# Performance work log

Measured on AMD Instinct MI355X. Metric: run time of the kernel, lower is better.

## Reference

```python
import jax, jax.numpy as jnp
import numpy as np

B = 262144
STATE_DIM = 12
ACTION_DIM = 1
MSG_DIM = 32
MAX_CHILDREN = 2
EPS = 1e-12  # F.normalize default eps


def _l2norm(x):
    n = jnp.sqrt(jnp.sum(x * x, axis=-1, keepdims=True))
    return x / jnp.maximum(n, EPS)


def setup_inputs() -> dict:
    key = jax.random.key(0)
    ks = jax.random.split(key, 16)

    def lin(kw, kb, out_d, in_d):
        lim = 1.0 / np.sqrt(in_d)
        w = jax.random.uniform(kw, (out_d, in_d), jnp.float32, -lim, lim)
        b = jax.random.uniform(kb, (out_d,), jnp.float32, -lim, lim)
        return w, b

    state = jax.random.normal(ks[0], (B, STATE_DIM), jnp.float32)
    action = jax.random.normal(ks[1], (B, ACTION_DIM), jnp.float32)

    # ModelUp (sNet): fc1, fc2, fc3
    up_w1, up_b1 = lin(ks[2], ks[3], 64, STATE_DIM + ACTION_DIM)
    up_w2, up_b2 = lin(ks[4], ks[5], 64, 64 + MSG_DIM * MAX_CHILDREN)
    up_w3, up_b3 = lin(ks[6], ks[7], MSG_DIM, 64)

    # ModelDownAction.model = MLPBase(msg_dim + action_dim + msg_dim, msg_dim)
    dyn_w1, dyn_b1 = lin(ks[8], ks[9], 400, MSG_DIM + ACTION_DIM + MSG_DIM)
    dyn_w2, dyn_b2 = lin(ks[10], ks[11], 300, 400)
    dyn_w3, dyn_b3 = lin(ks[12], ks[13], MSG_DIM, 300)

    return dict(state=state, action=action,
                up_w1=up_w1, up_b1=up_b1, up_w2=up_w2, up_b2=up_b2,
                up_w3=up_w3, up_b3=up_b3,
                dyn_w1=dyn_w1, dyn_b1=dyn_b1, dyn_w2=dyn_w2, dyn_b2=dyn_b2,
                dyn_w3=dyn_w3, dyn_b3=dyn_b3)


def reference(state, action,
              up_w1, up_b1, up_w2, up_b2, up_w3, up_b3,
              dyn_w1, dyn_b1, dyn_w2, dyn_b2, dyn_w3, dyn_b3):
    # num_limbs == 1, parents = [-1], td = bu = True, disable_fold = True
    x = state                              # (B, state_dim)
    u = action                             # (B, 1)

    # ---- bottom_up_transmission(0): ModelUp with all-zero child messages ----
    m_children = jnp.zeros((B, MSG_DIM * MAX_CHILDREN), x.dtype)
    xu = jnp.concatenate([x, u], axis=-1)
    xu = _l2norm(xu @ up_w1.T + up_b1)                       # (B, 64)
    xum = jnp.tanh(jnp.concatenate([xu, m_children], axis=-1))
    xum = jnp.tanh(xum @ up_w2.T + up_b2)                    # (B, 64)
    msg_up = _l2norm(xum @ up_w3.T + up_b3)                  # (B, msg_dim)

    # ---- top_down_transmission(0): ModelDownAction, state := msg_up ----
    # parent_msg = zeros, self_children_idx = 0 -> msg_in = zeros slice
    msg_in = jnp.zeros((B, MSG_DIM), x.dtype)
    xum2 = jnp.concatenate([msg_up, u, msg_in], axis=-1)     # (B, 2*msg_dim+1)
    h = jax.nn.relu(xum2 @ dyn_w1.T + dyn_b1)                # (B, 400)
    h = jax.nn.relu(h @ dyn_w2.T + dyn_b2)                   # (B, 300)
    delta = h @ dyn_w3.T + dyn_b3                            # (B, msg_dim)

    # stack over num_limbs=1 then squeeze -> (B, msg_dim)
    return delta
```

## Files before the change

kernel.cpp:

```cpp
#include <hip/hip_runtime.h>
#include <stdint.h>

typedef short s16x8 __attribute__((ext_vector_type(8)));
typedef float f32x16 __attribute__((ext_vector_type(16)));
typedef unsigned int u32;
typedef unsigned int u32x2 __attribute__((ext_vector_type(2)));

#define NFRAG 336
#define WS_USHORTS (NFRAG*512)
#define PANEL_FRAGS 14
#define PANEL_BYTES (PANEL_FRAGS*1024)
#define LDS_BYTES (3*PANEL_BYTES)

#define MFMA(a,b,c) __builtin_amdgcn_mfma_f32_32x32x16_bf16((a),(b),(c),0,0,0)

__device__ __forceinline__ unsigned short f2bf(float f){
  u32 x = __builtin_bit_cast(u32, f);
  x += 0x7fffu + ((x >> 16) & 1u);
  return (unsigned short)(x >> 16);
}

__device__ __forceinline__ float bfhi(float b){
  return __builtin_bit_cast(float, (u32)f2bf(b) << 16);
}

__device__ __forceinline__ u32 pkbf(float a, float b){
  u32 r;
  asm("v_cvt_pk_bf16_f32 %0, %1, %2" : "=v"(r) : "v"(a), "v"(b));
  return r;
}

__device__ __forceinline__ float fast_tanh(float x){
  float ax = fabsf(x);
  float e = __expf(-2.0f * ax);
  float r = (1.0f - e) * __builtin_amdgcn_rcpf(1.0f + e);
  return x < 0.0f ? -r : r;
}

__device__ __forceinline__ float halfsum(float s){
  return s + __shfl_xor(s, 32);
}

__device__ __forceinline__ void tile2frags(const f32x16 v, s16x8& f0, s16x8& f1){
  u32 w00 = pkbf(v[0],  v[1]),  w01 = pkbf(v[2],  v[3]);
  u32 w10 = pkbf(v[4],  v[5]),  w11 = pkbf(v[6],  v[7]);
  u32 w20 = pkbf(v[8],  v[9]),  w21 = pkbf(v[10], v[11]);
  u32 w30 = pkbf(v[12], v[13]), w31 = pkbf(v[14], v[15]);
  u32x2 p0 = __builtin_amdgcn_permlane32_swap(w00, w10, false, false);
  u32x2 p1 = __builtin_amdgcn_permlane32_swap(w01, w11, false, false);
  u32x2 p2 = __builtin_amdgcn_permlane32_swap(w20, w30, false, false);
  u32x2 p3 = __builtin_amdgcn_permlane32_swap(w21, w31, false, false);
  int4 r0, r1;
  r0.x = (int)p0[0]; r0.y = (int)p1[0]; r0.z = (int)p0[1]; r0.w = (int)p1[1];
  r1.x = (int)p2[0]; r1.y = (int)p3[0]; r1.z = (int)p2[1]; r1.w = (int)p3[1];
  f0 = __builtin_bit_cast(s16x8, r0);
  f1 = __builtin_bit_cast(s16x8, r1);
}

__global__ void wconv_kernel(const float* __restrict__ uw1, const float* __restrict__ ub1,
                             const float* __restrict__ uw2, const float* __restrict__ ub2,
                             const float* __restrict__ uw3, const float* __restrict__ ub3,
                             const float* __restrict__ dw1, const float* __restrict__ db1,
                             const float* __restrict__ dw2, const float* __restrict__ db2,
                             const float* __restrict__ dw3, const float* __restrict__ db3,
                             unsigned short* __restrict__ wp)
{
  int i = blockIdx.x*256 + threadIdx.x;
  if (i >= WS_USHORTS) return;
  int f    = i >> 9;
  int lane = (i >> 3) & 63;
  int j    = i & 7;
  int row  = lane & 31;
  int k8   = (lane >> 5)*8 + j;
  float v = 0.0f;
  if (f < 2){
    int feat = f*32 + row; int k = k8;
    if (k < 13) v = uw1[feat*13 + k];
    else if (k == 13) v = ub1[feat];
    else if (k == 14) v = ub1[feat] - bfhi(ub1[feat]);
  } else if (f < 12){
    int t = f - 2; int kt = t >> 1, nt = t & 1;
    int feat = nt*32 + row; int k = kt*16 + k8;
    if (k < 64) v = uw2[feat*128 + k];
    else if (k == 64) v = ub2[feat];
    else if (k == 65) v = ub2[feat] - bfhi(ub2[feat]);
  } else if (f < 17){
    int kt = f - 12; int feat = row; int k = kt*16 + k8;
    if (k < 64) v = uw3[feat*64 + k];
    else if (k == 64) v = ub3[feat];
    else if (k == 65) v = ub3[feat] - bfhi(ub3[feat]);
  } else if (f < 56){
    int t = f - 17; int nt = t/3, kt = t%3;
    int feat = nt*32 + row; int k = kt*16 + k8;
    if (feat < 400){
      if (k < 33) v = dw1[feat*65 + k];
      else if (k == 33) v = db1[feat];
      else if (k == 34) v = db1[feat] - bfhi(db1[feat]);
    } else if ((feat == 400 || feat == 401) && k == 33) v = 1.0f;
  } else {
    int t = f - 56; int n = t/56; int r = t%56;
    if (r < 52){
      int kf = r >> 1, nt = r & 1;
      int feat = n*64 + nt*32 + row; int k = kf*16 + k8;
      if (feat < 300){
        if (k < 400) v = dw2[feat*400 + k];
        else if (k == 400) v = db2[feat];
        else if (k == 401) v = db2[feat] - bfhi(db2[feat]);
      } else if ((feat == 300 || feat == 301) && k == 400) v = 1.0f;
    } else {
      int kt = n*4 + (r - 52); int feat = row; int k = kt*16 + k8;
      if (k < 300) v = dw3[feat*300 + k];
      else if (k == 300) v = db3[feat];
      else if (k == 301) v = db3[feat] - bfhi(db3[feat]);
    }
  }
  wp[i] = f2bf(v);
}

__device__ __forceinline__ s16x8 fragF(const char* sm, int f, int ln){
  return *(const s16x8*)(sm + ((f/PANEL_FRAGS) % 3)*PANEL_BYTES
                            + (f % PANEL_FRAGS)*1024 + ln*16);
}

__device__ __forceinline__ void stage14(const unsigned short* wp, char* sm, int panel, int tid){
  char* dst = sm + (panel % 3)*PANEL_BYTES;
  const char* src = (const char*)wp + (size_t)panel*PANEL_BYTES;
  #pragma unroll
  for (int j = 0; j < 3; ++j){
    int off = j*4096 + tid*16;
    __builtin_amdgcn_global_load_lds(
      (const __attribute__((address_space(1))) unsigned int*)(src + off),
      (__attribute__((address_space(3))) unsigned int*)(dst + off), 16, 0, 0);
  }
  int off3 = 12288 + (tid & 127)*16;
  __builtin_amdgcn_global_load_lds(
    (const __attribute__((address_space(1))) unsigned int*)(src + off3),
    (__attribute__((address_space(3))) unsigned int*)(dst + off3), 16, 0, 0);
}

#define BND(P) { \
  if ((P) >= 23) { asm volatile("s_waitcnt vmcnt(0) lgkmcnt(0)" ::: "memory"); } \
  else           { asm volatile("s_waitcnt vmcnt(4) lgkmcnt(0)" ::: "memory"); } \
  __builtin_amdgcn_s_barrier(); \
  __builtin_amdgcn_sched_barrier(0); \
  if ((P)+2 <= 23) stage14(wp, sm, (P)+2, tid); \
}

#define D1TRIPLE(f0_, oA, oB) { \
  f32x16 a = {}; \
  __builtin_amdgcn_s_setprio(1); \
  a = MFMA(fragF(sm, (f0_)+0, ln), mf0, a); \
  a = MFMA(fragF(sm, (f0_)+1, ln), mf1, a); \
  a = MFMA(fragF(sm, (f0_)+2, ln), mf2, a); \
  __builtin_amdgcn_s_setprio(0); \
  _Pragma("unroll") \
  for (int r = 0; r < 16; ++r) a[r] = fmaxf(a[r], 0.f); \
  tile2frags(a, oA, oB); }

#define D2RUN(fb, r0, r1) { \
  __builtin_amdgcn_s_setprio(1); \
  _Pragma("unroll") \
  for (int r = (r0); r < (r1); ++r){ \
    s16x8 hb = h1f[r>>1]; \
    if (r & 1) d2a1 = MFMA(fragF(sm, (fb)+r, ln), hb, d2a1); \
    else       d2a0 = MFMA(fragF(sm, (fb)+r, ln), hb, d2a0); \
  } \
  __builtin_amdgcn_s_setprio(0); }

#define D2TAIL(fb) { \
  _Pragma("unroll") \
  for (int r = 0; r < 16; ++r){ \
    d2a0[r] = fmaxf(d2a0[r], 0.f); \
    d2a1[r] = fmaxf(d2a1[r], 0.f); \
  } \
  s16x8 c0, c1, c2, c3; \
  tile2frags(d2a0, c0, c1); \
  tile2frags(d2a1, c2, c3); \
  __builtin_amdgcn_s_setprio(1); \
  acc3 = MFMA(fragF(sm, (fb)+52, ln), c0, acc3); \
  acc3 = MFMA(fragF(sm, (fb)+53, ln), c1, acc3); \
  acc3 = MFMA(fragF(sm, (fb)+54, ln), c2, acc3); \
  acc3 = MFMA(fragF(sm, (fb)+55, ln), c3, acc3); \
  __builtin_amdgcn_s_setprio(0); }

#define CHUNK(fb, P0) { \
  f32x16 d2a0 = {}, d2a1 = {}; \
  BND(P0) \
  D2RUN(fb, 0, 14) \
  BND((P0)+1) \
  D2RUN(fb, 14, 28) \
  BND((P0)+2) \
  D2RUN(fb, 28, 42) \
  BND((P0)+3) \
  D2RUN(fb, 42, 52) \
  D2TAIL(fb) \
}

__global__ __launch_bounds__(256, 2) void fused_kernel(
    const float* __restrict__ state, const float* __restrict__ action,
    const unsigned short* __restrict__ wp, float* __restrict__ out)
{
  __shared__ __align__(1024) char sm[LDS_BYTES];

  const int tid = threadIdx.x;
  const int ln  = tid & 63;
  const int wid = tid >> 6;
  const int c   = ln & 31;
  const int h   = ln >> 5;
  const int rowb = blockIdx.x*128 + wid*32;

  const float* xr = state + (size_t)(rowb + c)*12;
  float u = action[rowb + c];
  float4 xa, xbr;
  if (h == 0){
    xa  = *(const float4*)xr;
    xbr = *(const float4*)(xr + 4);
  } else {
    xa  = *(const float4*)(xr + 8);
  }

  stage14(wp, sm, 0, tid);
  stage14(wp, sm, 1, tid);
  BND(0)

  float4 xb = (h == 0) ? xbr : float4{u, 1.0f, 1.0f, 0.0f};
  int4 xw;
  xw.x = pkbf(xa.x, xa.y); xw.y = pkbf(xa.z, xa.w);
  xw.z = pkbf(xb.x, xb.y); xw.w = pkbf(xb.z, xb.w);
  s16x8 xfrag = __builtin_bit_cast(s16x8, xw);
  int4 ow = {0,0,0,0}; if (h == 0) ow.x = 0x3F803F80;
  s16x8 onef = __builtin_bit_cast(s16x8, ow);
  int4 mw = {0,0,0,0};
  if (h == 0){ mw.x = pkbf(u, 1.0f); mw.y = 0x3F80; }
  s16x8 mf2 = __builtin_bit_cast(s16x8, mw);

  s16x8 mf0, mf1;
  {
    s16x8 xf0, xf1, xf2, xf3, tf0, tf1, tf2, tf3;
    {
      f32x16 a0 = {}, a1 = {};
      a0 = MFMA(fragF(sm, 0, ln), xfrag, a0);
      a1 = MFMA(fragF(sm, 1, ln), xfrag, a1);
      float s = 0.f;
      #pragma unroll
      for (int r = 0; r < 16; ++r) s += a0[r]*a0[r] + a1[r]*a1[r];
      s = halfsum(s);
      float inv = __builtin_amdgcn_rsqf(fmaxf(s, 1e-24f));
      #pragma unroll
      for (int r = 0; r < 16; ++r){
        a0[r] = fast_tanh(a0[r]*inv);
        a1[r] = fast_tanh(a1[r]*inv);
      }
      tile2frags(a0, xf0, xf1);
      tile2frags(a1, xf2, xf3);
    }
    {
      f32x16 a0 = {}, a1 = {};
      __builtin_amdgcn_s_setprio(1);
      a0 = MFMA(fragF(sm, 2, ln), xf0, a0);  a1 = MFMA(fragF(sm, 3, ln), xf0, a1);
      a0 = MFMA(fragF(sm, 4, ln), xf1, a0);  a1 = MFMA(fragF(sm, 5, ln), xf1, a1);
      a0 = MFMA(fragF(sm, 6, ln), xf2, a0);  a1 = MFMA(fragF(sm, 7, ln), xf2, a1);
      a0 = MFMA(fragF(sm, 8, ln), xf3, a0);  a1 = MFMA(fragF(sm, 9, ln), xf3, a1);
      a0 = MFMA(fragF(sm,10, ln), onef, a0); a1 = MFMA(fragF(sm,11, ln), onef, a1);
      __builtin_amdgcn_s_setprio(0);
      #pragma unroll
      for (int r = 0; r < 16; ++r){
        a0[r] = fast_tanh(a0[r]);
        a1[r] = fast_tanh(a1[r]);
      }
      tile2frags(a0, tf0, tf1);
      tile2frags(a1, tf2, tf3);
    }
    {
      f32x16 m = {};
      __builtin_amdgcn_s_setprio(1);
      m = MFMA(fragF(sm,12, ln), tf0, m);
      m = MFMA(fragF(sm,13, ln), tf1, m);
      __builtin_amdgcn_s_setprio(0);
      BND(1)
      __builtin_amdgcn_s_setprio(1);
      m = MFMA(fragF(sm,14, ln), tf2, m);
      m = MFMA(fragF(sm,15, ln), tf3, m);
      m = MFMA(fragF(sm,16, ln), onef, m);
      __builtin_amdgcn_s_setprio(0);
      float s = 0.f;
      #pragma unroll
      for (int r = 0; r < 16; ++r) s += m[r]*m[r];
      s = halfsum(s);
      float inv = __builtin_amdgcn_rsqf(fmaxf(s, 1e-24f));
      #pragma unroll
      for (int r = 0; r < 16; ++r) m[r] *= inv;
      tile2frags(m, mf0, mf1);
    }
  }

  s16x8 h1f[26];
  D1TRIPLE(17, h1f[0],  h1f[1])
  D1TRIPLE(20, h1f[2],  h1f[3])
  D1TRIPLE(23, h1f[4],  h1f[5])
  {
    f32x16 a = {};
    __builtin_amdgcn_s_setprio(1);
    a = MFMA(fragF(sm, 26, ln), mf0, a);
    a = MFMA(fragF(sm, 27, ln), mf1, a);
    __builtin_amdgcn_s_setprio(0);
    BND(2)
    __builtin_amdgcn_s_setprio(1);
    a = MFMA(fragF(sm, 28, ln), mf2, a);
    __builtin_amdgcn_s_setprio(0);
    #pragma unroll
    for (int r = 0; r < 16; ++r) a[r] = fmaxf(a[r], 0.f);
    tile2frags(a, h1f[6], h1f[7]);
  }
  D1TRIPLE(29, h1f[8],  h1f[9])
  D1TRIPLE(32, h1f[10], h1f[11])
  D1TRIPLE(35, h1f[12], h1f[13])
  D1TRIPLE(38, h1f[14], h1f[15])
  {
    f32x16 a = {};
    __builtin_amdgcn_s_setprio(1);
    a = MFMA(fragF(sm, 41, ln), mf0, a);
    __builtin_amdgcn_s_setprio(0);
    BND(3)
    __builtin_amdgcn_s_setprio(1);
    a = MFMA(fragF(sm, 42, ln), mf1, a);
    a = MFMA(fragF(sm, 43, ln), mf2, a);
    __builtin_amdgcn_s_setprio(0);
    #pragma unroll
    for (int r = 0; r < 16; ++r) a[r] = fmaxf(a[r], 0.f);
    tile2frags(a, h1f[16], h1f[17]);
  }
  D1TRIPLE(44, h1f[18], h1f[19])
  D1TRIPLE(47, h1f[20], h1f[21])
  D1TRIPLE(50, h1f[22], h1f[23])
  D1TRIPLE(53, h1f[24], h1f[25])

  f32x16 acc3 = {};
  CHUNK(56,  4)
  CHUNK(112, 8)
  CHUNK(168, 12)
  CHUNK(224, 16)
  CHUNK(280, 20)

  float* op = out + (size_t)(rowb + c)*32;
  #pragma unroll
  for (int p = 0; p < 4; ++p){
    float4 v4 = {acc3[4*p+0], acc3[4*p+1], acc3[4*p+2], acc3[4*p+3]};
    *(float4*)(op + p*8 + h*4) = v4;
  }
}

extern "C" void kernel_launch(void* const* d_in, const int* in_sizes, int n_in,
                              void* d_out, int out_size, void* d_ws, size_t ws_size,
                              hipStream_t stream)
{
  const float* state  = (const float*)d_in[0];
  const float* action = (const float*)d_in[1];
  const float* up_w1  = (const float*)d_in[2];
  const float* up_b1  = (const float*)d_in[3];
  const float* up_w2  = (const float*)d_in[4];
  const float* up_b2  = (const float*)d_in[5];
  const float* up_w3  = (const float*)d_in[6];
  const float* up_b3  = (const float*)d_in[7];
  const float* dyn_w1 = (const float*)d_in[8];
  const float* dyn_b1 = (const float*)d_in[9];
  const float* dyn_w2 = (const float*)d_in[10];
  const float* dyn_b2 = (const float*)d_in[11];
  const float* dyn_w3 = (const float*)d_in[12];
  const float* dyn_b3 = (const float*)d_in[13];
  unsigned short* wp = (unsigned short*)d_ws;

  hipLaunchKernelGGL(wconv_kernel, dim3((WS_USHORTS + 255)/256), dim3(256), 0, stream,
                     up_w1, up_b1, up_w2, up_b2, up_w3, up_b3,
                     dyn_w1, dyn_b1, dyn_w2, dyn_b2, dyn_w3, dyn_b3, wp);
  hipLaunchKernelGGL(fused_kernel, dim3(262144/128), dim3(256), 0, stream,
                     state, action, wp, (float*)d_out);
}
```

Before: 94.16 us.

## Software-pipeline layer epilogues across MFMA chunks and simplify barrier waits

Layer-1 tiles now alternate between two accumulators, so each tile's ReLU and bf16 conversion overlaps the next tile's MFMAs. Layer-2 chunks double-buffer their accumulators, spreading the previous chunk's ReLU, conversion and layer-3 MFMAs across the next chunk's barrier phases. Layer-3 weights are preloaded into registers before their LDS panel is overwritten. The hand-tuned partial vmcnt waits are replaced by plain __syncthreads, which may wait on all outstanding prefetches and weaken load overlap; the extra live accumulators also raise register pressure at two blocks per CU.

```diff
diff --git a/kernel.cpp b/kernel.cpp
--- a/kernel.cpp
+++ b/kernel.cpp
@@ -139,61 +139,69 @@
 }
 
 #define BND(P) { \
-  if ((P) >= 23) { asm volatile("s_waitcnt vmcnt(0) lgkmcnt(0)" ::: "memory"); } \
-  else           { asm volatile("s_waitcnt vmcnt(4) lgkmcnt(0)" ::: "memory"); } \
-  __builtin_amdgcn_s_barrier(); \
-  __builtin_amdgcn_sched_barrier(0); \
+  __syncthreads(); \
   if ((P)+2 <= 23) stage14(wp, sm, (P)+2, tid); \
 }
 
-#define D1TRIPLE(f0_, oA, oB) { \
-  f32x16 a = {}; \
+#define TAIL1(aSrc, oA, oB) { \
+  _Pragma("unroll") \
+  for (int r = 0; r < 16; ++r) aSrc[r] = fmaxf(aSrc[r], 0.f); \
+  tile2frags(aSrc, oA, oB); }
+
+#define D1MM(f0_, acc) { \
   __builtin_amdgcn_s_setprio(1); \
-  a = MFMA(fragF(sm, (f0_)+0, ln), mf0, a); \
-  a = MFMA(fragF(sm, (f0_)+1, ln), mf1, a); \
-  a = MFMA(fragF(sm, (f0_)+2, ln), mf2, a); \
-  __builtin_amdgcn_s_setprio(0); \
-  _Pragma("unroll") \
-  for (int r = 0; r < 16; ++r) a[r] = fmaxf(a[r], 0.f); \
-  tile2frags(a, oA, oB); }
-
-#define D2RUN(fb, r0, r1) { \
+  acc = MFMA(fragF(sm, (f0_)+0, ln), mf0, acc); \
+  acc = MFMA(fragF(sm, (f0_)+1, ln), mf1, acc); \
+  acc = MFMA(fragF(sm, (f0_)+2, ln), mf2, acc); \
+  __builtin_amdgcn_s_setprio(0); }
+
+#define D2R(fb, r0, r1, A0, A1) { \
   __builtin_amdgcn_s_setprio(1); \
   _Pragma("unroll") \
   for (int r = (r0); r < (r1); ++r){ \
     s16x8 hb = h1f[r>>1]; \
-    if (r & 1) d2a1 = MFMA(fragF(sm, (fb)+r, ln), hb, d2a1); \
-    else       d2a0 = MFMA(fragF(sm, (fb)+r, ln), hb, d2a0); \
+    if (r & 1) A1 = MFMA(fragF(sm, (fb)+r, ln), hb, A1); \
+    else       A0 = MFMA(fragF(sm, (fb)+r, ln), hb, A0); \
   } \
   __builtin_amdgcn_s_setprio(0); }
 
-#define D2TAIL(fb) { \
+#define LOADD3W(fb) { \
+  d3w0 = fragF(sm, (fb)+52, ln); \
+  d3w1 = fragF(sm, (fb)+53, ln); \
+  d3w2 = fragF(sm, (fb)+54, ln); \
+  d3w3 = fragF(sm, (fb)+55, ln); }
+
+#define TAILD2_RELU(A0, A1) { \
   _Pragma("unroll") \
   for (int r = 0; r < 16; ++r){ \
-    d2a0[r] = fmaxf(d2a0[r], 0.f); \
-    d2a1[r] = fmaxf(d2a1[r], 0.f); \
-  } \
-  s16x8 c0, c1, c2, c3; \
-  tile2frags(d2a0, c0, c1); \
-  tile2frags(d2a1, c2, c3); \
+    A0[r] = fmaxf(A0[r], 0.f); \
+    A1[r] = fmaxf(A1[r], 0.f); \
+  } }
+#define TAILD2_CVT(A0, A1) { \
+  tile2frags(A0, cT0, cT1); \
+  tile2frags(A1, cT2, cT3); }
+#define TAILD2_D3() { \
   __builtin_amdgcn_s_setprio(1); \
-  acc3 = MFMA(fragF(sm, (fb)+52, ln), c0, acc3); \
-  acc3 = MFMA(fragF(sm, (fb)+53, ln), c1, acc3); \
-  acc3 = MFMA(fragF(sm, (fb)+54, ln), c2, acc3); \
-  acc3 = MFMA(fragF(sm, (fb)+55, ln), c3, acc3); \
+  acc3 = MFMA(d3w0, cT0, acc3); \
+  acc3 = MFMA(d3w1, cT1, acc3); \
+  acc3 = MFMA(d3w2, cT2, acc3); \
+  acc3 = MFMA(d3w3, cT3, acc3); \
   __builtin_amdgcn_s_setprio(0); }
 
-#define CHUNK(fb, P0) { \
-  f32x16 d2a0 = {}, d2a1 = {}; \
+#define CHUNKN(fb, P0, C0_, C1_, PR0, PR1) { \
   BND(P0) \
-  D2RUN(fb, 0, 14) \
+  C0_ = vzero; C1_ = vzero; \
+  D2R(fb, 0, 14, C0_, C1_) \
+  TAILD2_RELU(PR0, PR1) \
   BND((P0)+1) \
-  D2RUN(fb, 14, 28) \
+  D2R(fb, 14, 28, C0_, C1_) \
+  TAILD2_CVT(PR0, PR1) \
   BND((P0)+2) \
-  D2RUN(fb, 28, 42) \
+  D2R(fb, 28, 42, C0_, C1_) \
+  TAILD2_D3() \
   BND((P0)+3) \
-  D2RUN(fb, 42, 52) \
-  D2TAIL(fb) \
+  D2R(fb, 42, 52, C0_, C1_) \
+  LOADD3W(fb) \
 }
 
 __global__ __launch_bounds__(256, 2) void fused_kernel(
@@ -208,6 +216,8 @@
   const int c   = ln & 31;
   const int h   = ln >> 5;
   const int rowb = blockIdx.x*128 + wid*32;
+
+  const f32x16 vzero = {};
 
   const float* xr = state + (size_t)(rowb + c)*12;
   float u = action[rowb + c];
@@ -295,52 +305,63 @@
   }
 
   s16x8 h1f[26];
-  D1TRIPLE(17, h1f[0],  h1f[1])
-  D1TRIPLE(20, h1f[2],  h1f[3])
-  D1TRIPLE(23, h1f[4],  h1f[5])
+  f32x16 aX = vzero, aY = vzero;
+  D1MM(17, aX)
+  D1MM(20, aY)  TAIL1(aX, h1f[0],  h1f[1])
+  aX = vzero; D1MM(23, aX)  TAIL1(aY, h1f[2],  h1f[3])
+  aY = vzero;
+  __builtin_amdgcn_s_setprio(1);
+  aY = MFMA(fragF(sm, 26, ln), mf0, aY);
+  aY = MFMA(fragF(sm, 27, ln), mf1, aY);
+  __builtin_amdgcn_s_setprio(0);
+  BND(2)
+  __builtin_amdgcn_s_setprio(1);
+  aY = MFMA(fragF(sm, 28, ln), mf2, aY);
+  __builtin_amdgcn_s_setprio(0);
+  TAIL1(aX, h1f[4], h1f[5])
+  aX = vzero; D1MM(29, aX)  TAIL1(aY, h1f[6],  h1f[7])
+  aY = vzero; D1MM(32, aY)  TAIL1(aX, h1f[8],  h1f[9])
+  aX = vzero; D1MM(35, aX)  TAIL1(aY, h1f[10], h1f[11])
+  aY = vzero; D1MM(38, aY)  TAIL1(aX, h1f[12], h1f[13])
+  aX = vzero;
+  __builtin_amdgcn_s_setprio(1);
+  aX = MFMA(fragF(sm, 41, ln), mf0, aX);
+  __builtin_amdgcn_s_setprio(0);
+  BND(3)
+  __builtin_amdgcn_s_setprio(1);
+  aX = MFMA(fragF(sm, 42, ln), mf1, aX);
+  aX = MFMA(fragF(sm, 43, ln), mf2, aX);
+  __builtin_amdgcn_s_setprio(0);
+  TAIL1(aY, h1f[14], h1f[15])
+  aY = vzero; D1MM(44, aY)  TAIL1(aX, h1f[16], h1f[17])
+  aX = vzero; D1MM(47, aX)  TAIL1(aY, h1f[18], h1f[19])
+  aY = vzero; D1MM(50, aY)  TAIL1(aX, h1f[20], h1f[21])
+  aX = vzero; D1MM(53, aX)  TAIL1(aY, h1f[22], h1f[23])
+
+  f32x16 acc3 = vzero;
+  f32x16 dA0, dA1, dB0, dB1;
+  s16x8 d3w0, d3w1, d3w2, d3w3, cT0, cT1, cT2, cT3;
+
   {
-    f32x16 a = {};
-    __builtin_amdgcn_s_setprio(1);
-    a = MFMA(fragF(sm, 26, ln), mf0, a);
-    a = MFMA(fragF(sm, 27, ln), mf1, a);
-    __builtin_amdgcn_s_setprio(0);
-    BND(2)
-    __builtin_amdgcn_s_setprio(1);
-    a = MFMA(fragF(sm, 28, ln), mf2, a);
-    __builtin_amdgcn_s_setprio(0);
-    #pragma unroll
-    for (int r = 0; r < 16; ++r) a[r] = fmaxf(a[r], 0.f);
-    tile2frags(a, h1f[6], h1f[7]);
-  }
-  D1TRIPLE(29, h1f[8],  h1f[9])
-  D1TRIPLE(32, h1f[10], h1f[11])
-  D1TRIPLE(35, h1f[12], h1f[13])
-  D1TRIPLE(38, h1f[14], h1f[15])
-  {
-    f32x16 a = {};
-    __builtin_amdgcn_s_setprio(1);
-    a = MFMA(fragF(sm, 41, ln), mf0, a);
-    __builtin_amdgcn_s_setprio(0);
-    BND(3)
-    __builtin_amdgcn_s_setprio(1);
-    a = MFMA(fragF(sm, 42, ln), mf1, a);
-    a = MFMA(fragF(sm, 43, ln), mf2, a);
-    __builtin_amdgcn_s_setprio(0);
-    #pragma unroll
-    for (int r = 0; r < 16; ++r) a[r] = fmaxf(a[r], 0.f);
-    tile2frags(a, h1f[16], h1f[17]);
-  }
-  D1TRIPLE(44, h1f[18], h1f[19])
-  D1TRIPLE(47, h1f[20], h1f[21])
-  D1TRIPLE(50, h1f[22], h1f[23])
-  D1TRIPLE(53, h1f[24], h1f[25])
-
-  f32x16 acc3 = {};
-  CHUNK(56,  4)
-  CHUNK(112, 8)
-  CHUNK(168, 12)
-  CHUNK(224, 16)
-  CHUNK(280, 20)
+    BND(4)
+    dA0 = vzero; dA1 = vzero;
+    D2R(56, 0, 14, dA0, dA1)
+    TAIL1(aX, h1f[24], h1f[25])
+    BND(5)
+    D2R(56, 14, 28, dA0, dA1)
+    BND(6)
+    D2R(56, 28, 42, dA0, dA1)
+    BND(7)
+    D2R(56, 42, 52, dA0, dA1)
+    LOADD3W(56)
+  }
+  CHUNKN(112,  8, dB0, dB1, dA0, dA1)
+  CHUNKN(168, 12, dA0, dA1, dB0, dB1)
+  CHUNKN(224, 16, dB0, dB1, dA0, dA1)
+  CHUNKN(280, 20, dA0, dA1, dB0, dB1)
+  TAILD2_RELU(dA0, dA1)
+  TAILD2_CVT(dA0, dA1)
+  TAILD2_D3()
 
   float* op = out + (size_t)(rowb + c)*32;
   #pragma unroll
```

After: 92.42 us. Within noise of the previous version (-1.8%).

## Shrink weight panels to 8 fragments and raise occupancy to three blocks per CU

Applied to the files above, without the earlier changes.

Cuts the LDS staging panels from 14 to 8 fragments so the triple-buffered LDS footprint drops from 42KB to 24KB, and raises launch bounds to 3 blocks per CU. The panel boundaries are redistributed across the layer-1 and layer-2 compute, giving 42 panels instead of 24. The last h1 fragment (always the bias-one pattern) is replaced by the constant onef to save registers. The explicit vmcnt-based wait is replaced by plain __syncthreads. The cost is more barriers per block and tighter register budgets, which could cause spills.

```diff
diff --git a/kernel.cpp b/kernel.cpp
--- a/kernel.cpp
+++ b/kernel.cpp
@@ -8,7 +8,7 @@
 
 #define NFRAG 336
 #define WS_USHORTS (NFRAG*512)
-#define PANEL_FRAGS 14
+#define PANEL_FRAGS 8
 #define PANEL_BYTES (PANEL_FRAGS*1024)
 #define LDS_BYTES (3*PANEL_BYTES)
 
@@ -122,81 +122,80 @@
                             + (f % PANEL_FRAGS)*1024 + ln*16);
 }
 
-__device__ __forceinline__ void stage14(const unsigned short* wp, char* sm, int panel, int tid){
+__device__ __forceinline__ void stage8(const unsigned short* wp, char* sm, int panel, int tid){
   char* dst = sm + (panel % 3)*PANEL_BYTES;
   const char* src = (const char*)wp + (size_t)panel*PANEL_BYTES;
   #pragma unroll
-  for (int j = 0; j < 3; ++j){
+  for (int j = 0; j < 2; ++j){
     int off = j*4096 + tid*16;
     __builtin_amdgcn_global_load_lds(
       (const __attribute__((address_space(1))) unsigned int*)(src + off),
       (__attribute__((address_space(3))) unsigned int*)(dst + off), 16, 0, 0);
   }
-  int off3 = 12288 + (tid & 127)*16;
-  __builtin_amdgcn_global_load_lds(
-    (const __attribute__((address_space(1))) unsigned int*)(src + off3),
-    (__attribute__((address_space(3))) unsigned int*)(dst + off3), 16, 0, 0);
 }
 
 #define BND(P) { \
-  if ((P) >= 23) { asm volatile("s_waitcnt vmcnt(0) lgkmcnt(0)" ::: "memory"); } \
-  else           { asm volatile("s_waitcnt vmcnt(4) lgkmcnt(0)" ::: "memory"); } \
-  __builtin_amdgcn_s_barrier(); \
-  __builtin_amdgcn_sched_barrier(0); \
-  if ((P)+2 <= 23) stage14(wp, sm, (P)+2, tid); \
-}
-
-#define D1TRIPLE(f0_, oA, oB) { \
-  f32x16 a = {}; \
+  __syncthreads(); \
+  if ((P)+2 <= 41) stage8(wp, sm, (P)+2, tid); \
+}
+
+#define TAIL1(aSrc, oA, oB) { \
+  _Pragma("unroll") \
+  for (int r = 0; r < 16; ++r) aSrc[r] = fmaxf(aSrc[r], 0.f); \
+  tile2frags(aSrc, oA, oB); }
+
+#define D1MM(f0_, acc) { \
   __builtin_amdgcn_s_setprio(1); \
-  a = MFMA(fragF(sm, (f0_)+0, ln), mf0, a); \
-  a = MFMA(fragF(sm, (f0_)+1, ln), mf1, a); \
-  a = MFMA(fragF(sm, (f0_)+2, ln), mf2, a); \
-  __builtin_amdgcn_s_setprio(0); \
-  _Pragma("unroll") \
-  for (int r = 0; r < 16; ++r) a[r] = fmaxf(a[r], 0.f); \
-  tile2frags(a, oA, oB); }
-
-#define D2RUN(fb, r0, r1) { \
+  acc = MFMA(fragF(sm, (f0_)+0, ln), mf0, acc); \
+  acc = MFMA(fragF(sm, (f0_)+1, ln), mf1, acc); \
+  acc = MFMA(fragF(sm, (f0_)+2, ln), mf2, acc); \
+  __builtin_amdgcn_s_setprio(0); }
+
+#define D2R(fb, r0, r1) { \
   __builtin_amdgcn_s_setprio(1); \
   _Pragma("unroll") \
   for (int r = (r0); r < (r1); ++r){ \
-    s16x8 hb = h1f[r>>1]; \
+    s16x8 hb = ((r>>1) == 25) ? onef : h1f[r>>1]; \
     if (r & 1) d2a1 = MFMA(fragF(sm, (fb)+r, ln), hb, d2a1); \
     else       d2a0 = MFMA(fragF(sm, (fb)+r, ln), hb, d2a0); \
   } \
   __builtin_amdgcn_s_setprio(0); }
 
-#define D2TAIL(fb) { \
-  _Pragma("unroll") \
-  for (int r = 0; r < 16; ++r){ \
-    d2a0[r] = fmaxf(d2a0[r], 0.f); \
-    d2a1[r] = fmaxf(d2a1[r], 0.f); \
+#define CHUNKS(fb, P0) { \
+  BND(P0) \
+  d2a0 = vzero; d2a1 = vzero; \
+  D2R(fb, 0, 8) \
+  BND((P0)+1) \
+  D2R(fb, 8, 16) \
+  BND((P0)+2) \
+  D2R(fb, 16, 24) \
+  BND((P0)+3) \
+  D2R(fb, 24, 32) \
+  BND((P0)+4) \
+  D2R(fb, 32, 40) \
+  BND((P0)+5) \
+  D2R(fb, 40, 48) \
+  BND((P0)+6) \
+  D2R(fb, 48, 52) \
+  { \
+    _Pragma("unroll") \
+    for (int r = 0; r < 16; ++r){ \
+      d2a0[r] = fmaxf(d2a0[r], 0.f); \
+      d2a1[r] = fmaxf(d2a1[r], 0.f); \
+    } \
+    s16x8 c0, c1, c2, c3; \
+    tile2frags(d2a0, c0, c1); \
+    tile2frags(d2a1, c2, c3); \
+    __builtin_amdgcn_s_setprio(1); \
+    acc3 = MFMA(fragF(sm, (fb)+52, ln), c0, acc3); \
+    acc3 = MFMA(fragF(sm, (fb)+53, ln), c1, acc3); \
+    acc3 = MFMA(fragF(sm, (fb)+54, ln), c2, acc3); \
+    acc3 = MFMA(fragF(sm, (fb)+55, ln), c3, acc3); \
+    __builtin_amdgcn_s_setprio(0); \
   } \
-  s16x8 c0, c1, c2, c3; \
-  tile2frags(d2a0, c0, c1); \
-  tile2frags(d2a1, c2, c3); \
-  __builtin_amdgcn_s_setprio(1); \
-  acc3 = MFMA(fragF(sm, (fb)+52, ln), c0, acc3); \
-  acc3 = MFMA(fragF(sm, (fb)+53, ln), c1, acc3); \
-  acc3 = MFMA(fragF(sm, (fb)+54, ln), c2, acc3); \
-  acc3 = MFMA(fragF(sm, (fb)+55, ln), c3, acc3); \
-  __builtin_amdgcn_s_setprio(0); }
-
-#define CHUNK(fb, P0) { \
-  f32x16 d2a0 = {}, d2a1 = {}; \
-  BND(P0) \
-  D2RUN(fb, 0, 14) \
-  BND((P0)+1) \
-  D2RUN(fb, 14, 28) \
-  BND((P0)+2) \
-  D2RUN(fb, 28, 42) \
-  BND((P0)+3) \
-  D2RUN(fb, 42, 52) \
-  D2TAIL(fb) \
-}
-
-__global__ __launch_bounds__(256, 2) void fused_kernel(
+}
+
+__global__ __launch_bounds__(256, 3) void fused_kernel(
     const float* __restrict__ state, const float* __restrict__ action,
     const unsigned short* __restrict__ wp, float* __restrict__ out)
 {
@@ -208,6 +207,8 @@
   const int c   = ln & 31;
   const int h   = ln >> 5;
   const int rowb = blockIdx.x*128 + wid*32;
+
+  const f32x16 vzero = {};
 
   const float* xr = state + (size_t)(rowb + c)*12;
   float u = action[rowb + c];
@@ -219,8 +220,8 @@
     xa  = *(const float4*)(xr + 8);
   }
 
-  stage14(wp, sm, 0, tid);
-  stage14(wp, sm, 1, tid);
+  stage8(wp, sm, 0, tid);
+  stage8(wp, sm, 1, tid);
   BND(0)
 
   float4 xb = (h == 0) ? xbr : float4{u, 1.0f, 1.0f, 0.0f};
@@ -260,6 +261,9 @@
       a0 = MFMA(fragF(sm, 2, ln), xf0, a0);  a1 = MFMA(fragF(sm, 3, ln), xf0, a1);
       a0 = MFMA(fragF(sm, 4, ln), xf1, a0);  a1 = MFMA(fragF(sm, 5, ln), xf1, a1);
       a0 = MFMA(fragF(sm, 6, ln), xf2, a0);  a1 = MFMA(fragF(sm, 7, ln), xf2, a1);
+      __builtin_amdgcn_s_setprio(0);
+      BND(1)
+      __builtin_amdgcn_s_setprio(1);
       a0 = MFMA(fragF(sm, 8, ln), xf3, a0);  a1 = MFMA(fragF(sm, 9, ln), xf3, a1);
       a0 = MFMA(fragF(sm,10, ln), onef, a0); a1 = MFMA(fragF(sm,11, ln), onef, a1);
       __builtin_amdgcn_s_setprio(0);
@@ -276,11 +280,11 @@
       __builtin_amdgcn_s_setprio(1);
       m = MFMA(fragF(sm,12, ln), tf0, m);
       m = MFMA(fragF(sm,13, ln), tf1, m);
-      __builtin_amdgcn_s_setprio(0);
-      BND(1)
-      __builtin_amdgcn_s_setprio(1);
       m = MFMA(fragF(sm,14, ln), tf2, m);
       m = MFMA(fragF(sm,15, ln), tf3, m);
+      __builtin_amdgcn_s_setprio(0);
+      BND(2)
+      __builtin_amdgcn_s_setprio(1);
       m = MFMA(fragF(sm,16, ln), onef, m);
       __builtin_amdgcn_s_setprio(0);
       float s = 0.f;
@@ -294,53 +298,64 @@
     }
   }
 
-  s16x8 h1f[26];
-  D1TRIPLE(17, h1f[0],  h1f[1])
-  D1TRIPLE(20, h1f[2],  h1f[3])
-  D1TRIPLE(23, h1f[4],  h1f[5])
+  s16x8 h1f[25];
   {
-    f32x16 a = {};
-    __builtin_amdgcn_s_setprio(1);
-    a = MFMA(fragF(sm, 26, ln), mf0, a);
-    a = MFMA(fragF(sm, 27, ln), mf1, a);
-    __builtin_amdgcn_s_setprio(0);
-    BND(2)
-    __builtin_amdgcn_s_setprio(1);
-    a = MFMA(fragF(sm, 28, ln), mf2, a);
-    __builtin_amdgcn_s_setprio(0);
-    #pragma unroll
-    for (int r = 0; r < 16; ++r) a[r] = fmaxf(a[r], 0.f);
-    tile2frags(a, h1f[6], h1f[7]);
-  }
-  D1TRIPLE(29, h1f[8],  h1f[9])
-  D1TRIPLE(32, h1f[10], h1f[11])
-  D1TRIPLE(35, h1f[12], h1f[13])
-  D1TRIPLE(38, h1f[14], h1f[15])
-  {
-    f32x16 a = {};
-    __builtin_amdgcn_s_setprio(1);
-    a = MFMA(fragF(sm, 41, ln), mf0, a);
+    f32x16 a;
+    a = vzero; D1MM(17, a)  TAIL1(a, h1f[0],  h1f[1])
+    a = vzero; D1MM(20, a)  TAIL1(a, h1f[2],  h1f[3])
+    a = vzero;
+    __builtin_amdgcn_s_setprio(1);
+    a = MFMA(fragF(sm, 23, ln), mf0, a);
     __builtin_amdgcn_s_setprio(0);
     BND(3)
     __builtin_amdgcn_s_setprio(1);
-    a = MFMA(fragF(sm, 42, ln), mf1, a);
-    a = MFMA(fragF(sm, 43, ln), mf2, a);
-    __builtin_amdgcn_s_setprio(0);
-    #pragma unroll
-    for (int r = 0; r < 16; ++r) a[r] = fmaxf(a[r], 0.f);
-    tile2frags(a, h1f[16], h1f[17]);
-  }
-  D1TRIPLE(44, h1f[18], h1f[19])
-  D1TRIPLE(47, h1f[20], h1f[21])
-  D1TRIPLE(50, h1f[22], h1f[23])
-  D1TRIPLE(53, h1f[24], h1f[25])
-
-  f32x16 acc3 = {};
-  CHUNK(56,  4)
-  CHUNK(112, 8)
-  CHUNK(168, 12)
-  CHUNK(224, 16)
-  CHUNK(280, 20)
+    a = MFMA(fragF(sm, 24, ln), mf1, a);
+    a = MFMA(fragF(sm, 25, ln), mf2, a);
+    __builtin_amdgcn_s_setprio(0);
+    TAIL1(a, h1f[4], h1f[5])
+    a = vzero; D1MM(26, a)  TAIL1(a, h1f[6],  h1f[7])
+    a = vzero; D1MM(29, a)  TAIL1(a, h1f[8],  h1f[9])
+    BND(4)
+    a = vzero; D1MM(32, a)  TAIL1(a, h1f[10], h1f[11])
+    a = vzero; D1MM(35, a)  TAIL1(a, h1f[12], h1f[13])
+    a = vzero;
+    __builtin_amdgcn_s_setprio(1);
+    a = MFMA(fragF(sm, 38, ln), mf0, a);
+    a = MFMA(fragF(sm, 39, ln), mf1, a);
+    __builtin_amdgcn_s_setprio(0);
+    BND(5)
+    __builtin_amdgcn_s_setprio(1);
+    a = MFMA(fragF(sm, 40, ln), mf2, a);
+    __builtin_amdgcn_s_setprio(0);
+    TAIL1(a, h1f[14], h1f[15])
+    a = vzero; D1MM(41, a)  TAIL1(a, h1f[16], h1f[17])
+    a = vzero; D1MM(44, a)  TAIL1(a, h1f[18], h1f[19])
+    a = vzero;
+    __builtin_amdgcn_s_setprio(1);
+    a = MFMA(fragF(sm, 47, ln), mf0, a);
+    __builtin_amdgcn_s_setprio(0);
+    BND(6)
+    __builtin_amdgcn_s_setprio(1);
+    a = MFMA(fragF(sm, 48, ln), mf1, a);
+    a = MFMA(fragF(sm, 49, ln), mf2, a);
+    __builtin_amdgcn_s_setprio(0);
+    TAIL1(a, h1f[20], h1f[21])
+    a = vzero; D1MM(50, a)  TAIL1(a, h1f[22], h1f[23])
+    a = vzero; D1MM(53, a)
+    {
+      s16x8 dumm;
+      TAIL1(a, h1f[24], dumm)
+      (void)dumm;
+    }
+  }
+
+  f32x16 acc3 = vzero;
+  f32x16 d2a0, d2a1;
+  CHUNKS(56,  7)
+  CHUNKS(112, 14)
+  CHUNKS(168, 21)
+  CHUNKS(224, 28)
+  CHUNKS(280, 35)
 
   float* op = out + (size_t)(rowb + c)*32;
   #pragma unroll
```

Result: slower. 115.9 us (+23.1%).
